# Optimization experiments

Hardware: AMD Instinct MI355X
Metric: run time of the kernel (lower is better)

## Reference

```python
import jax, jax.numpy as jnp
import numpy as np

N, F_IN, R, H, U, B, E = 20000, 256, 8, 4, 64, 4, 320000
NEG_SLOPE = 0.2  # torch F.leaky_relu default is 0.01, but GAT/RGAT uses 0.2; source uses F.leaky_relu -> 0.01
LRELU_SLOPE = 0.01


def setup_inputs() -> dict:
    key = jax.random.key(0)
    ks = jax.random.split(key, 8)
    x = jax.random.normal(ks[0], (N, F_IN), dtype=jnp.float32)
    basis = jax.random.normal(ks[1], (B, F_IN, U), dtype=jnp.float32) * 0.05
    coeff = jax.random.normal(ks[2], (R * H, B), dtype=jnp.float32)
    attn_q = jax.random.normal(ks[3], (R, H, U), dtype=jnp.float32) * 0.1
    attn_k = jax.random.normal(ks[4], (R, H, U), dtype=jnp.float32) * 0.1
    src = jax.random.randint(ks[5], (E,), 0, N, dtype=jnp.int32)
    dst = jax.random.randint(ks[6], (E,), 0, N, dtype=jnp.int32)
    rel = jax.random.randint(ks[7], (E,), 0, R, dtype=jnp.int32)
    return {"x": x, "basis": basis, "coeff": coeff, "attn_q": attn_q,
            "attn_k": attn_k, "src": src, "dst": dst, "rel": rel}


def reference(x, basis, coeff, attn_q, attn_k, src, dst, rel):
    n = x.shape[0]
    # Basis-decomposed relational kernels: W_{r,h} = sum_b c_{(r,h),b} W'_b
    W = jnp.einsum("cb,bfu->cfu", coeff, basis).reshape(R, H, F_IN, U)
    # Relation/head-specific projections: [N, R, H, U]
    xp = jnp.einsum("nf,rhfu->nrhu", x, W)
    # GAT-style 'sum' attention, attention_units=1: scalar query/key per (node, r, h)
    q = jnp.einsum("nrhu,rhu->nrh", xp, attn_q)  # [N, R, H]
    k = jnp.einsum("nrhu,rhu->nrh", xp, attn_k)  # [N, R, H]
    # Per-edge logits, gathered along sparse support: [E, H]
    logit = jax.nn.leaky_relu(q[src, rel] + k[dst, rel], negative_slope=LRELU_SLOPE)
    # ARGAT: segment softmax per destination node across all relations/edges
    m = jax.ops.segment_max(logit, dst, num_segments=n)        # [N, H]
    m = jnp.where(jnp.isfinite(m), m, 0.0)
    ex = jnp.exp(logit - m[dst])                               # [E, H]
    denom = jax.ops.segment_sum(ex, dst, num_segments=n)       # [N, H]
    alpha = ex / jnp.maximum(denom[dst], 1e-16)                # [E, H]
    # Weighted scatter-aggregation of messages: [N, H, U]
    msg = xp[src, rel] * alpha[:, :, None]                     # [E, H, U]
    out = jax.ops.segment_sum(msg, dst, num_segments=n)
    # head_aggregation='mean', activation=None, use_bias=False
    return out.mean(axis=1)  # [N, U]
```

## Files before the change

### kernel.cpp

```cpp
#include <hip/hip_runtime.h>
#include <hip/hip_bf16.h>
#include <math.h>

#define F_IN    256
#define R_REL   8
#define H_HEADS 4
#define U_DIM   64
#define B_BASES 4
#define C_TOT   (R_REL * H_HEADS)
#define LRELU   0.01f
#define SLOT_CAP 64

typedef __attribute__((ext_vector_type(8))) short short8;
typedef __attribute__((ext_vector_type(4))) float f32x4;

__device__ __forceinline__ unsigned short f2bf(float f) {
    unsigned int u = __float_as_uint(f);
    u = (u + 0x7FFF + ((u >> 16) & 1)) >> 16;
    return (unsigned short)u;
}
__device__ __forceinline__ float bf2f_lo(unsigned int v) { return __uint_as_float(v << 16); }
__device__ __forceinline__ float bf2f_hi(unsigned int v) { return __uint_as_float(v & 0xFFFF0000u); }

__global__ __launch_bounds__(256) void prep_all(const float* __restrict__ x,
                                                unsigned short* __restrict__ xb,
                                                int total4,
                                                int* __restrict__ counts,
                                                int n_nodes,
                                                const float* __restrict__ basis,
                                                const float* __restrict__ coeff,
                                                const float* __restrict__ attn_q,
                                                const float* __restrict__ attn_k,
                                                unsigned short* __restrict__ Wt,
                                                int n_cast_blocks) {
    if (blockIdx.x < (unsigned)n_cast_blocks) {
        int i = blockIdx.x * 256 + threadIdx.x;
        if (i < n_nodes) counts[i] = 0;
        if (i >= total4) return;
        float4 v = *(const float4*)&x[(size_t)i * 4];
        ushort4 o;
        o.x = f2bf(v.x); o.y = f2bf(v.y); o.z = f2bf(v.z); o.w = f2bf(v.w);
        *(ushort4*)&xb[(size_t)i * 4] = o;
        return;
    }

    __shared__ float aq[64], ak[64];
    int c = blockIdx.x - n_cast_blocks;
    int f = threadIdx.x;
    if (f < 64) {
        aq[f] = attn_q[c * 64 + f];
        ak[f] = attn_k[c * 64 + f];
    }
    __syncthreads();

    #pragma unroll
    for (int j = 0; j < 8; ++j) {
        int nn = c * 8 + j;
        int b = nn & 3, u = nn >> 2;
        Wt[(size_t)nn * 256 + f] = f2bf(basis[(size_t)b * (F_IN * U_DIM) + (size_t)f * U_DIM + u]);
    }

    float sq = 0.f, sk = 0.f;
    #pragma unroll
    for (int b = 0; b < B_BASES; ++b) {
        float cb = coeff[c * 4 + b];
        const float* bp = basis + (size_t)b * (F_IN * U_DIM) + (size_t)f * U_DIM;
        float dq = 0.f, dk = 0.f;
        #pragma unroll
        for (int u = 0; u < 64; ++u) {
            float v = bp[u];
            dq += v * aq[u];
            dk += v * ak[u];
        }
        sq += cb * dq;
        sk += cb * dk;
    }
    Wt[(size_t)(256 + c) * 256 + f] = f2bf(sq);
    Wt[(size_t)(288 + c) * 256 + f] = f2bf(sk);
}

__global__ __launch_bounds__(256) void gemm_scatter(const unsigned short* __restrict__ xb,
                                                    const unsigned short* __restrict__ Wt,
                                                    unsigned short* __restrict__ zb,
                                                    float* __restrict__ qk,
                                                    const int* __restrict__ src,
                                                    const int* __restrict__ dst,
                                                    const int* __restrict__ rel,
                                                    int* __restrict__ counts,
                                                    unsigned int* __restrict__ slots,
                                                    int nrows, int E) {
    if (blockIdx.y == 5) {
        int stride = gridDim.x * 256;
        int base = blockIdx.x * 256 + threadIdx.x;
        #pragma unroll
        for (int j = 0; j < 8; ++j) {
            int i = base + j * stride;
            if (i < E) {
                int d = dst[i];
                int pos = atomicAdd(&counts[d], 1);
                if (pos < SLOT_CAP)
                    slots[(size_t)d * SLOT_CAP + pos] = (unsigned)src[i] | ((unsigned)rel[i] << 20);
            }
        }
        return;
    }

    __shared__ unsigned short Al[128 * 72];
    __shared__ unsigned short Bl[64 * 72];

    const int tid  = threadIdx.x;
    const int wave = tid >> 6;
    const int lane = tid & 63;
    const int wr   = wave >> 1;
    const int wc   = wave & 1;
    const int m0   = blockIdx.x * 128;
    const int bb   = blockIdx.y;
    const int l15  = lane & 15;
    const int quad = lane >> 4;

    f32x4 acc[4][2];
    #pragma unroll
    for (int t = 0; t < 4; ++t)
        #pragma unroll
        for (int s = 0; s < 2; ++s)
            acc[t][s] = (f32x4){0.f, 0.f, 0.f, 0.f};

    for (int k0 = 0; k0 < 256; k0 += 64) {
        #pragma unroll
        for (int p = 0; p < 4; ++p) {
            int idx = p * 256 + tid;
            int row = idx >> 3;
            int cg  = idx & 7;
            int gr  = m0 + row;
            uint4 v = make_uint4(0, 0, 0, 0);
            if (gr < nrows) v = *(const uint4*)&xb[(size_t)gr * 256 + k0 + cg * 8];
            *(uint4*)&Al[row * 72 + cg * 8] = v;
        }
        #pragma unroll
        for (int p = 0; p < 2; ++p) {
            int idx = p * 256 + tid;
            int row = idx >> 3;
            int cg  = idx & 7;
            uint4 v = *(const uint4*)&Wt[(size_t)(bb * 64 + row) * 256 + k0 + cg * 8];
            *(uint4*)&Bl[row * 72 + cg * 8] = v;
        }
        __syncthreads();

        #pragma unroll
        for (int ks = 0; ks < 64; ks += 32) {
            short8 bfr[2];
            #pragma unroll
            for (int s = 0; s < 2; ++s)
                bfr[s] = *(short8*)&Bl[(wc * 32 + s * 16 + l15) * 72 + ks + quad * 8];
            #pragma unroll
            for (int t = 0; t < 4; ++t) {
                short8 afr = *(short8*)&Al[(wr * 64 + t * 16 + l15) * 72 + ks + quad * 8];
                #pragma unroll
                for (int s = 0; s < 2; ++s)
                    acc[t][s] = __builtin_amdgcn_mfma_f32_16x16x32_bf16(afr, bfr[s], acc[t][s], 0, 0, 0);
            }
        }
        __syncthreads();
    }

    #pragma unroll
    for (int t = 0; t < 4; ++t) {
        #pragma unroll
        for (int s = 0; s < 2; ++s) {
            int c_local = wc * 32 + s * 16 + l15;
            #pragma unroll
            for (int reg = 0; reg < 4; ++reg) {
                int m = m0 + wr * 64 + t * 16 + quad * 4 + reg;
                if (m < nrows) {
                    float v = acc[t][s][reg];
                    if (bb < 4) zb[(size_t)m * 256 + bb * 64 + c_local] = f2bf(v);
                    else        qk[(size_t)m * 64 + c_local] = v;
                }
            }
        }
    }
}

__global__ __launch_bounds__(256) void agg_kernel(const unsigned short* __restrict__ zb,
                                                  const float* __restrict__ qk,
                                                  const float* __restrict__ coeff,
                                                  const unsigned int* __restrict__ slots,
                                                  const int* __restrict__ counts,
                                                  float* __restrict__ out,
                                                  int n_nodes) {
    __shared__ float cf[128];
    __shared__ float4 gsh[4][64];
    __shared__ int    ssh[4][64];
    if (threadIdx.x < 128) cf[threadIdx.x] = coeff[threadIdx.x];
    __syncthreads();

    int wv   = threadIdx.x >> 6;
    int n    = blockIdx.x * 4 + wv;
    int lane = threadIdx.x & 63;
    if (n >= n_nodes) return;

    int cnt = counts[n];
    if (cnt > SLOT_CAP) cnt = SLOT_CAP;
    const unsigned int* sl = slots + (size_t)n * SLOT_CAP;

    float e0 = 0.f, e1 = 0.f, e2 = 0.f, e3 = 0.f;
    int s_edge = 0, r_edge = 0;
    if (lane < cnt) {
        unsigned p = sl[lane];
        s_edge = (int)(p & 0xFFFFFu);
        r_edge = (int)(p >> 20);
        float4 q  = *(const float4*)&qk[(size_t)s_edge * 64 + r_edge * 4];
        float4 kv = *(const float4*)&qk[(size_t)n * 64 + 32 + r_edge * 4];
        float l0 = q.x + kv.x, l1 = q.y + kv.y, l2 = q.z + kv.z, l3 = q.w + kv.w;
        l0 = (l0 > 0.f) ? l0 : LRELU * l0;
        l1 = (l1 > 0.f) ? l1 : LRELU * l1;
        l2 = (l2 > 0.f) ? l2 : LRELU * l2;
        l3 = (l3 > 0.f) ? l3 : LRELU * l3;
        e0 = __expf(l0); e1 = __expf(l1); e2 = __expf(l2); e3 = __expf(l3);
    }
    float d0 = e0, d1 = e1, d2 = e2, d3 = e3;
    #pragma unroll
    for (int off = 32; off; off >>= 1) {
        d0 += __shfl_xor(d0, off);
        d1 += __shfl_xor(d1, off);
        d2 += __shfl_xor(d2, off);
        d3 += __shfl_xor(d3, off);
    }
    if (lane < cnt) {
        float a0 = e0 * ((d0 > 0.f) ? 0.25f / d0 : 0.f);
        float a1 = e1 * ((d1 > 0.f) ? 0.25f / d1 : 0.f);
        float a2 = e2 * ((d2 > 0.f) ? 0.25f / d2 : 0.f);
        float a3 = e3 * ((d3 > 0.f) ? 0.25f / d3 : 0.f);
        const float* c0 = &cf[(r_edge * 4 + 0) * 4];
        const float* c1 = &cf[(r_edge * 4 + 1) * 4];
        const float* c2 = &cf[(r_edge * 4 + 2) * 4];
        const float* c3 = &cf[(r_edge * 4 + 3) * 4];
        float4 g4;
        g4.x = a0 * c0[0] + a1 * c1[0] + a2 * c2[0] + a3 * c3[0];
        g4.y = a0 * c0[1] + a1 * c1[1] + a2 * c2[1] + a3 * c3[1];
        g4.z = a0 * c0[2] + a1 * c1[2] + a2 * c2[2] + a3 * c3[2];
        g4.w = a0 * c0[3] + a1 * c1[3] + a2 * c2[3] + a3 * c3[3];
        gsh[wv][lane] = g4;
        ssh[wv][lane] = s_edge;
    }

    int es = lane >> 3;
    int g  = lane & 7;
    float acc[4][2];
    #pragma unroll
    for (int v = 0; v < 4; ++v) { acc[v][0] = 0.f; acc[v][1] = 0.f; }

    for (int base = 0; base < cnt; base += 8) {
        int i = base + es;
        if (i < cnt) {
            float4 g4 = gsh[wv][i];
            int s = ssh[wv][i];
            const unsigned short* zr = zb + (size_t)s * 256 + g * 8;
            #pragma unroll
            for (int v = 0; v < 4; ++v) {
                uint4 z4 = *(const uint4*)(zr + v * 64);
                acc[v][0] += g4.x * bf2f_lo(z4.x) + g4.y * bf2f_hi(z4.x) +
                             g4.z * bf2f_lo(z4.y) + g4.w * bf2f_hi(z4.y);
                acc[v][1] += g4.x * bf2f_lo(z4.z) + g4.y * bf2f_hi(z4.z) +
                             g4.z * bf2f_lo(z4.w) + g4.w * bf2f_hi(z4.w);
            }
        }
    }

    #pragma unroll
    for (int v = 0; v < 4; ++v) {
        #pragma unroll
        for (int j = 0; j < 2; ++j) {
            acc[v][j] += __shfl_xor(acc[v][j], 8);
            acc[v][j] += __shfl_xor(acc[v][j], 16);
            acc[v][j] += __shfl_xor(acc[v][j], 32);
        }
    }
    if (es == 0) {
        #pragma unroll
        for (int v = 0; v < 4; ++v) {
            float2 o = make_float2(acc[v][0], acc[v][1]);
            *(float2*)&out[(size_t)n * 64 + v * 16 + g * 2] = o;
        }
    }
}

extern "C" void kernel_launch(void* const* d_in, const int* in_sizes, int n_in,
                              void* d_out, int out_size, void* d_ws, size_t ws_size,
                              hipStream_t stream) {
    const float* x      = (const float*)d_in[0];
    const float* basis  = (const float*)d_in[1];
    const float* coeff  = (const float*)d_in[2];
    const float* attn_q = (const float*)d_in[3];
    const float* attn_k = (const float*)d_in[4];
    const int*   src    = (const int*)d_in[5];
    const int*   dst    = (const int*)d_in[6];
    const int*   rel    = (const int*)d_in[7];
    float* out = (float*)d_out;

    const int n_nodes = in_sizes[0] / F_IN;
    const int E       = in_sizes[5];

    char* ws = (char*)d_ws;
    size_t off = 0;
    auto alloc = [&](size_t bytes) -> void* {
        void* p = ws + off;
        off += bytes;
        off = (off + 255) & ~(size_t)255;
        return p;
    };
    unsigned short* xb   = (unsigned short*)alloc((size_t)n_nodes * 256 * 2);
    unsigned short* Wt   = (unsigned short*)alloc((size_t)320 * 256 * 2);
    unsigned short* zb   = (unsigned short*)alloc((size_t)n_nodes * 256 * 2);
    float* qk            = (float*)alloc((size_t)n_nodes * 64 * 4);
    unsigned int* slots  = (unsigned int*)alloc((size_t)n_nodes * SLOT_CAP * 4);
    int* counts          = (int*)alloc((size_t)n_nodes * 4);

    const int total4 = n_nodes * 64;
    const int n_cast_blocks = (total4 + 255) / 256;

    prep_all<<<n_cast_blocks + C_TOT, 256, 0, stream>>>(
        x, xb, total4, counts, n_nodes, basis, coeff, attn_q, attn_k, Wt, n_cast_blocks);

    dim3 g2((n_nodes + 127) / 128, 6);
    gemm_scatter<<<g2, 256, 0, stream>>>(xb, Wt, zb, qk, src, dst, rel, counts, slots,
                                         n_nodes, E);

    agg_kernel<<<(n_nodes + 3) / 4, 256, 0, stream>>>(zb, qk, coeff, slots, counts, out, n_nodes);
}
```

Baseline: 139.5 us.

## Load MFMA operands directly from global memory instead of staging through LDS

Drops the shared-memory tiles and the __syncthreads barriers in the projection GEMM. Each wave now loads its A and B MFMA fragments straight from global memory via per-row pointers, with the K loop fully unrolled. This removes LDS write/read traffic and block barriers and frees LDS for occupancy. The cost is that A rows are re-read by both column waves and B by both row waves through the cache, and each lane issues 16-byte strided global loads rather than coalesced tile loads.

```diff
diff --git a/kernel.cpp b/kernel.cpp
--- a/kernel.cpp
+++ b/kernel.cpp
@@ -105,9 +105,6 @@
         return;
     }
 
-    __shared__ unsigned short Al[128 * 72];
-    __shared__ unsigned short Bl[64 * 72];
-
     const int tid  = threadIdx.x;
     const int wave = tid >> 6;
     const int lane = tid & 63;
@@ -118,6 +115,16 @@
     const int l15  = lane & 15;
     const int quad = lane >> 4;
 
+    const unsigned short* Aptr[4];
+    #pragma unroll
+    for (int t = 0; t < 4; ++t) {
+        int m = m0 + wr * 64 + t * 16 + l15;
+        if (m >= nrows) m = 0;
+        Aptr[t] = xb + (size_t)m * 256 + quad * 8;
+    }
+    const unsigned short* Bptr0 = Wt + (size_t)(bb * 64 + wc * 32 + l15) * 256 + quad * 8;
+    const unsigned short* Bptr1 = Bptr0 + 16 * 256;
+
     f32x4 acc[4][2];
     #pragma unroll
     for (int t = 0; t < 4; ++t)
@@ -125,42 +132,16 @@
         for (int s = 0; s < 2; ++s)
             acc[t][s] = (f32x4){0.f, 0.f, 0.f, 0.f};
 
-    for (int k0 = 0; k0 < 256; k0 += 64) {
-        #pragma unroll
-        for (int p = 0; p < 4; ++p) {
-            int idx = p * 256 + tid;
-            int row = idx >> 3;
-            int cg  = idx & 7;
-            int gr  = m0 + row;
-            uint4 v = make_uint4(0, 0, 0, 0);
-            if (gr < nrows) v = *(const uint4*)&xb[(size_t)gr * 256 + k0 + cg * 8];
-            *(uint4*)&Al[row * 72 + cg * 8] = v;
-        }
-        #pragma unroll
-        for (int p = 0; p < 2; ++p) {
-            int idx = p * 256 + tid;
-            int row = idx >> 3;
-            int cg  = idx & 7;
-            uint4 v = *(const uint4*)&Wt[(size_t)(bb * 64 + row) * 256 + k0 + cg * 8];
-            *(uint4*)&Bl[row * 72 + cg * 8] = v;
-        }
-        __syncthreads();
-
-        #pragma unroll
-        for (int ks = 0; ks < 64; ks += 32) {
-            short8 bfr[2];
-            #pragma unroll
-            for (int s = 0; s < 2; ++s)
-                bfr[s] = *(short8*)&Bl[(wc * 32 + s * 16 + l15) * 72 + ks + quad * 8];
-            #pragma unroll
-            for (int t = 0; t < 4; ++t) {
-                short8 afr = *(short8*)&Al[(wr * 64 + t * 16 + l15) * 72 + ks + quad * 8];
-                #pragma unroll
-                for (int s = 0; s < 2; ++s)
-                    acc[t][s] = __builtin_amdgcn_mfma_f32_16x16x32_bf16(afr, bfr[s], acc[t][s], 0, 0, 0);
-            }
-        }
-        __syncthreads();
+    #pragma unroll
+    for (int kk = 0; kk < 256; kk += 32) {
+        short8 b0 = *(const short8*)(Bptr0 + kk);
+        short8 b1 = *(const short8*)(Bptr1 + kk);
+        #pragma unroll
+        for (int t = 0; t < 4; ++t) {
+            short8 a = *(const short8*)(Aptr[t] + kk);
+            acc[t][0] = __builtin_amdgcn_mfma_f32_16x16x32_bf16(a, b0, acc[t][0], 0, 0, 0);
+            acc[t][1] = __builtin_amdgcn_mfma_f32_16x16x32_bf16(a, b1, acc[t][1], 0, 0, 0);
+        }
     }
 
     #pragma unroll
```

Result: slower. 145.7 us (+4.4%).

## Widen GEMM N-tile to 128, vectorize stores, fold edge scatter into qk blocks

Applied to the files above, without the earlier changes.

Changes the grid from 6 to 3 y-slices. The z projection now uses 128-column tiles (two y-slices instead of four), which halves how often the x tile is reloaded from global memory. The qk y-slice also runs the edge bucketing scatter after its GEMM. MFMA operands are swapped so each lane holds four consecutive output columns, which allows vectorized ushort4 and float4 stores. The trade-offs are higher register and LDS use, and serializing the scatter behind the qk GEMM, which lengthens those blocks and may make the load imbalanced.

```diff
diff --git a/kernel.cpp b/kernel.cpp
--- a/kernel.cpp
+++ b/kernel.cpp
@@ -79,34 +79,18 @@
     Wt[(size_t)(288 + c) * 256 + f] = f2bf(sk);
 }
 
-__global__ __launch_bounds__(256) void gemm_scatter(const unsigned short* __restrict__ xb,
-                                                    const unsigned short* __restrict__ Wt,
-                                                    unsigned short* __restrict__ zb,
-                                                    float* __restrict__ qk,
-                                                    const int* __restrict__ src,
-                                                    const int* __restrict__ dst,
-                                                    const int* __restrict__ rel,
-                                                    int* __restrict__ counts,
-                                                    unsigned int* __restrict__ slots,
-                                                    int nrows, int E) {
-    if (blockIdx.y == 5) {
-        int stride = gridDim.x * 256;
-        int base = blockIdx.x * 256 + threadIdx.x;
-        #pragma unroll
-        for (int j = 0; j < 8; ++j) {
-            int i = base + j * stride;
-            if (i < E) {
-                int d = dst[i];
-                int pos = atomicAdd(&counts[d], 1);
-                if (pos < SLOT_CAP)
-                    slots[(size_t)d * SLOT_CAP + pos] = (unsigned)src[i] | ((unsigned)rel[i] << 20);
-            }
-        }
-        return;
-    }
-
+__global__ __launch_bounds__(256) void gemm_fused(const unsigned short* __restrict__ xb,
+                                                  const unsigned short* __restrict__ Wt,
+                                                  unsigned short* __restrict__ zb,
+                                                  float* __restrict__ qk,
+                                                  const int* __restrict__ src,
+                                                  const int* __restrict__ dst,
+                                                  const int* __restrict__ rel,
+                                                  int* __restrict__ counts,
+                                                  unsigned int* __restrict__ slots,
+                                                  int nrows, int E) {
     __shared__ unsigned short Al[128 * 72];
-    __shared__ unsigned short Bl[64 * 72];
+    __shared__ unsigned short Bl[128 * 72];
 
     const int tid  = threadIdx.x;
     const int wave = tid >> 6;
@@ -118,65 +102,135 @@
     const int l15  = lane & 15;
     const int quad = lane >> 4;
 
-    f32x4 acc[4][2];
-    #pragma unroll
-    for (int t = 0; t < 4; ++t)
-        #pragma unroll
-        for (int s = 0; s < 2; ++s)
-            acc[t][s] = (f32x4){0.f, 0.f, 0.f, 0.f};
-
-    for (int k0 = 0; k0 < 256; k0 += 64) {
-        #pragma unroll
-        for (int p = 0; p < 4; ++p) {
-            int idx = p * 256 + tid;
-            int row = idx >> 3;
-            int cg  = idx & 7;
-            int gr  = m0 + row;
-            uint4 v = make_uint4(0, 0, 0, 0);
-            if (gr < nrows) v = *(const uint4*)&xb[(size_t)gr * 256 + k0 + cg * 8];
-            *(uint4*)&Al[row * 72 + cg * 8] = v;
-        }
-        #pragma unroll
-        for (int p = 0; p < 2; ++p) {
-            int idx = p * 256 + tid;
-            int row = idx >> 3;
-            int cg  = idx & 7;
-            uint4 v = *(const uint4*)&Wt[(size_t)(bb * 64 + row) * 256 + k0 + cg * 8];
-            *(uint4*)&Bl[row * 72 + cg * 8] = v;
-        }
-        __syncthreads();
-
-        #pragma unroll
-        for (int ks = 0; ks < 64; ks += 32) {
-            short8 bfr[2];
+    if (bb < 2) {
+        f32x4 acc[4][4];
+        #pragma unroll
+        for (int t = 0; t < 4; ++t)
+            #pragma unroll
+            for (int s = 0; s < 4; ++s)
+                acc[t][s] = (f32x4){0.f, 0.f, 0.f, 0.f};
+
+        for (int k0 = 0; k0 < 256; k0 += 64) {
+            #pragma unroll
+            for (int p = 0; p < 4; ++p) {
+                int idx = p * 256 + tid;
+                int row = idx >> 3;
+                int cg  = idx & 7;
+                int gr  = m0 + row;
+                uint4 v = make_uint4(0, 0, 0, 0);
+                if (gr < nrows) v = *(const uint4*)&xb[(size_t)gr * 256 + k0 + cg * 8];
+                *(uint4*)&Al[row * 72 + cg * 8] = v;
+            }
+            #pragma unroll
+            for (int p = 0; p < 4; ++p) {
+                int idx = p * 256 + tid;
+                int row = idx >> 3;
+                int cg  = idx & 7;
+                uint4 v = *(const uint4*)&Wt[(size_t)(bb * 128 + row) * 256 + k0 + cg * 8];
+                *(uint4*)&Bl[row * 72 + cg * 8] = v;
+            }
+            __syncthreads();
+
+            #pragma unroll
+            for (int ks = 0; ks < 64; ks += 32) {
+                short8 wf[4];
+                #pragma unroll
+                for (int s = 0; s < 4; ++s)
+                    wf[s] = *(short8*)&Bl[(wc * 64 + s * 16 + l15) * 72 + ks + quad * 8];
+                #pragma unroll
+                for (int t = 0; t < 4; ++t) {
+                    short8 xf = *(short8*)&Al[(wr * 64 + t * 16 + l15) * 72 + ks + quad * 8];
+                    #pragma unroll
+                    for (int s = 0; s < 4; ++s)
+                        acc[t][s] = __builtin_amdgcn_mfma_f32_16x16x32_bf16(wf[s], xf, acc[t][s], 0, 0, 0);
+                }
+            }
+            __syncthreads();
+        }
+
+        #pragma unroll
+        for (int t = 0; t < 4; ++t) {
+            int m = m0 + wr * 64 + t * 16 + l15;
+            if (m < nrows) {
+                #pragma unroll
+                for (int s = 0; s < 4; ++s) {
+                    int c = bb * 128 + wc * 64 + s * 16 + quad * 4;
+                    ushort4 o;
+                    o.x = f2bf(acc[t][s][0]);
+                    o.y = f2bf(acc[t][s][1]);
+                    o.z = f2bf(acc[t][s][2]);
+                    o.w = f2bf(acc[t][s][3]);
+                    *(ushort4*)&zb[(size_t)m * 256 + c] = o;
+                }
+            }
+        }
+    } else {
+        f32x4 acc[4][2];
+        #pragma unroll
+        for (int t = 0; t < 4; ++t)
             #pragma unroll
             for (int s = 0; s < 2; ++s)
-                bfr[s] = *(short8*)&Bl[(wc * 32 + s * 16 + l15) * 72 + ks + quad * 8];
-            #pragma unroll
-            for (int t = 0; t < 4; ++t) {
-                short8 afr = *(short8*)&Al[(wr * 64 + t * 16 + l15) * 72 + ks + quad * 8];
+                acc[t][s] = (f32x4){0.f, 0.f, 0.f, 0.f};
+
+        for (int k0 = 0; k0 < 256; k0 += 64) {
+            #pragma unroll
+            for (int p = 0; p < 4; ++p) {
+                int idx = p * 256 + tid;
+                int row = idx >> 3;
+                int cg  = idx & 7;
+                int gr  = m0 + row;
+                uint4 v = make_uint4(0, 0, 0, 0);
+                if (gr < nrows) v = *(const uint4*)&xb[(size_t)gr * 256 + k0 + cg * 8];
+                *(uint4*)&Al[row * 72 + cg * 8] = v;
+            }
+            #pragma unroll
+            for (int p = 0; p < 2; ++p) {
+                int idx = p * 256 + tid;
+                int row = idx >> 3;
+                int cg  = idx & 7;
+                uint4 v = *(const uint4*)&Wt[(size_t)(256 + row) * 256 + k0 + cg * 8];
+                *(uint4*)&Bl[row * 72 + cg * 8] = v;
+            }
+            __syncthreads();
+
+            #pragma unroll
+            for (int ks = 0; ks < 64; ks += 32) {
+                short8 wf[2];
                 #pragma unroll
                 for (int s = 0; s < 2; ++s)
-                    acc[t][s] = __builtin_amdgcn_mfma_f32_16x16x32_bf16(afr, bfr[s], acc[t][s], 0, 0, 0);
-            }
-        }
-        __syncthreads();
-    }
-
-    #pragma unroll
-    for (int t = 0; t < 4; ++t) {
-        #pragma unroll
-        for (int s = 0; s < 2; ++s) {
-            int c_local = wc * 32 + s * 16 + l15;
-            #pragma unroll
-            for (int reg = 0; reg < 4; ++reg) {
-                int m = m0 + wr * 64 + t * 16 + quad * 4 + reg;
-                if (m < nrows) {
-                    float v = acc[t][s][reg];
-                    if (bb < 4) zb[(size_t)m * 256 + bb * 64 + c_local] = f2bf(v);
-                    else        qk[(size_t)m * 64 + c_local] = v;
+                    wf[s] = *(short8*)&Bl[(wc * 32 + s * 16 + l15) * 72 + ks + quad * 8];
+                #pragma unroll
+                for (int t = 0; t < 4; ++t) {
+                    short8 xf = *(short8*)&Al[(wr * 64 + t * 16 + l15) * 72 + ks + quad * 8];
+                    #pragma unroll
+                    for (int s = 0; s < 2; ++s)
+                        acc[t][s] = __builtin_amdgcn_mfma_f32_16x16x32_bf16(wf[s], xf, acc[t][s], 0, 0, 0);
                 }
             }
+            __syncthreads();
+        }
+
+        #pragma unroll
+        for (int t = 0; t < 4; ++t) {
+            int m = m0 + wr * 64 + t * 16 + l15;
+            if (m < nrows) {
+                #pragma unroll
+                for (int s = 0; s < 2; ++s) {
+                    int c = wc * 32 + s * 16 + quad * 4;
+                    float4 o = make_float4(acc[t][s][0], acc[t][s][1],
+                                           acc[t][s][2], acc[t][s][3]);
+                    *(float4*)&qk[(size_t)m * 64 + c] = o;
+                }
+            }
+        }
+
+        int stride = gridDim.x * 256;
+        int base = blockIdx.x * 256 + tid;
+        for (int i = base; i < E; i += stride) {
+            int d = dst[i];
+            int pos = atomicAdd(&counts[d], 1);
+            if (pos < SLOT_CAP)
+                slots[(size_t)d * SLOT_CAP + pos] = (unsigned)src[i] | ((unsigned)rel[i] << 20);
         }
     }
 }
@@ -322,9 +376,9 @@
     prep_all<<<n_cast_blocks + C_TOT, 256, 0, stream>>>(
         x, xb, total4, counts, n_nodes, basis, coeff, attn_q, attn_k, Wt, n_cast_blocks);
 
-    dim3 g2((n_nodes + 127) / 128, 6);
-    gemm_scatter<<<g2, 256, 0, stream>>>(xb, Wt, zb, qk, src, dst, rel, counts, slots,
-                                         n_nodes, E);
+    dim3 g2((n_nodes + 127) / 128, 3);
+    gemm_fused<<<g2, 256, 0, stream>>>(xb, Wt, zb, qk, src, dst, rel, counts, slots,
+                                       n_nodes, E);
 
     agg_kernel<<<(n_nodes + 3) / 4, 256, 0, stream>>>(zb, qk, coeff, slots, counts, out, n_nodes);
 }
```

New measurement: 146.4 us. +4.9%, slower.

## Split aggregation into two column-half passes with buffered edge weights

Applied to the files above, without the earlier changes.

The aggregation kernel is split into two launches. The first computes the softmax-derived per-edge basis weights, stores them to a global buffer, and accumulates output columns 0-31. The second reuses those stored weights to accumulate columns 32-63. This halves the gathered row footprint per pass, which is meant to improve cache locality of the zb gathers. In exchange it adds an extra launch, a global weight buffer written and re-read, and a second pass over the slot indices.

```diff
diff --git a/kernel.cpp b/kernel.cpp
--- a/kernel.cpp
+++ b/kernel.cpp
@@ -181,11 +181,12 @@
     }
 }
 
-__global__ __launch_bounds__(256) void agg_kernel(const unsigned short* __restrict__ zb,
+__global__ __launch_bounds__(256) void agg_phase0(const unsigned short* __restrict__ zb,
                                                   const float* __restrict__ qk,
                                                   const float* __restrict__ coeff,
                                                   const unsigned int* __restrict__ slots,
                                                   const int* __restrict__ counts,
+                                                  float4* __restrict__ gbuf,
                                                   float* __restrict__ out,
                                                   int n_nodes) {
     __shared__ float cf[128];
@@ -242,13 +243,13 @@
         g4.w = a0 * c0[3] + a1 * c1[3] + a2 * c2[3] + a3 * c3[3];
         gsh[wv][lane] = g4;
         ssh[wv][lane] = s_edge;
+        gbuf[(size_t)n * SLOT_CAP + lane] = g4;
     }
 
     int es = lane >> 3;
     int g  = lane & 7;
-    float acc[4][2];
-    #pragma unroll
-    for (int v = 0; v < 4; ++v) { acc[v][0] = 0.f; acc[v][1] = 0.f; }
+    float acc[2][2];
+    acc[0][0] = acc[0][1] = acc[1][0] = acc[1][1] = 0.f;
 
     for (int base = 0; base < cnt; base += 8) {
         int i = base + es;
@@ -257,7 +258,7 @@
             int s = ssh[wv][i];
             const unsigned short* zr = zb + (size_t)s * 256 + g * 8;
             #pragma unroll
-            for (int v = 0; v < 4; ++v) {
+            for (int v = 0; v < 2; ++v) {
                 uint4 z4 = *(const uint4*)(zr + v * 64);
                 acc[v][0] += g4.x * bf2f_lo(z4.x) + g4.y * bf2f_hi(z4.x) +
                              g4.z * bf2f_lo(z4.y) + g4.w * bf2f_hi(z4.y);
@@ -268,7 +269,7 @@
     }
 
     #pragma unroll
-    for (int v = 0; v < 4; ++v) {
+    for (int v = 0; v < 2; ++v) {
         #pragma unroll
         for (int j = 0; j < 2; ++j) {
             acc[v][j] += __shfl_xor(acc[v][j], 8);
@@ -278,9 +279,65 @@
     }
     if (es == 0) {
         #pragma unroll
-        for (int v = 0; v < 4; ++v) {
+        for (int v = 0; v < 2; ++v) {
             float2 o = make_float2(acc[v][0], acc[v][1]);
             *(float2*)&out[(size_t)n * 64 + v * 16 + g * 2] = o;
+        }
+    }
+}
+
+__global__ __launch_bounds__(256) void agg_phase1(const unsigned short* __restrict__ zb,
+                                                  const unsigned int* __restrict__ slots,
+                                                  const int* __restrict__ counts,
+                                                  const float4* __restrict__ gbuf,
+                                                  float* __restrict__ out,
+                                                  int n_nodes) {
+    int wv   = threadIdx.x >> 6;
+    int n    = blockIdx.x * 4 + wv;
+    int lane = threadIdx.x & 63;
+    if (n >= n_nodes) return;
+
+    int cnt = counts[n];
+    if (cnt > SLOT_CAP) cnt = SLOT_CAP;
+    const unsigned int* sl = slots + (size_t)n * SLOT_CAP;
+    const float4* gb = gbuf + (size_t)n * SLOT_CAP;
+
+    int es = lane >> 3;
+    int g  = lane & 7;
+    float acc[2][2];
+    acc[0][0] = acc[0][1] = acc[1][0] = acc[1][1] = 0.f;
+
+    for (int base = 0; base < cnt; base += 8) {
+        int i = base + es;
+        if (i < cnt) {
+            float4 g4 = gb[i];
+            int s = (int)(sl[i] & 0xFFFFFu);
+            const unsigned short* zr = zb + (size_t)s * 256 + 128 + g * 8;
+            #pragma unroll
+            for (int v = 0; v < 2; ++v) {
+                uint4 z4 = *(const uint4*)(zr + v * 64);
+                acc[v][0] += g4.x * bf2f_lo(z4.x) + g4.y * bf2f_hi(z4.x) +
+                             g4.z * bf2f_lo(z4.y) + g4.w * bf2f_hi(z4.y);
+                acc[v][1] += g4.x * bf2f_lo(z4.z) + g4.y * bf2f_hi(z4.z) +
+                             g4.z * bf2f_lo(z4.w) + g4.w * bf2f_hi(z4.w);
+            }
+        }
+    }
+
+    #pragma unroll
+    for (int v = 0; v < 2; ++v) {
+        #pragma unroll
+        for (int j = 0; j < 2; ++j) {
+            acc[v][j] += __shfl_xor(acc[v][j], 8);
+            acc[v][j] += __shfl_xor(acc[v][j], 16);
+            acc[v][j] += __shfl_xor(acc[v][j], 32);
+        }
+    }
+    if (es == 0) {
+        #pragma unroll
+        for (int v = 0; v < 2; ++v) {
+            float2 o = make_float2(acc[v][0], acc[v][1]);
+            *(float2*)&out[(size_t)n * 64 + 32 + v * 16 + g * 2] = o;
         }
     }
 }
@@ -314,6 +371,7 @@
     unsigned short* zb   = (unsigned short*)alloc((size_t)n_nodes * 256 * 2);
     float* qk            = (float*)alloc((size_t)n_nodes * 64 * 4);
     unsigned int* slots  = (unsigned int*)alloc((size_t)n_nodes * SLOT_CAP * 4);
+    float4* gbuf         = (float4*)alloc((size_t)n_nodes * SLOT_CAP * 16);
     int* counts          = (int*)alloc((size_t)n_nodes * 4);
 
     const int total4 = n_nodes * 64;
@@ -326,5 +384,7 @@
     gemm_scatter<<<g2, 256, 0, stream>>>(xb, Wt, zb, qk, src, dst, rel, counts, slots,
                                          n_nodes, E);
 
-    agg_kernel<<<(n_nodes + 3) / 4, 256, 0, stream>>>(zb, qk, coeff, slots, counts, out, n_nodes);
-}
+    agg_phase0<<<(n_nodes + 3) / 4, 256, 0, stream>>>(zb, qk, coeff, slots, counts,
+                                                      gbuf, out, n_nodes);
+    agg_phase1<<<(n_nodes + 3) / 4, 256, 0, stream>>>(zb, slots, counts, gbuf, out, n_nodes);
+}
```

New measurement: 143.0 us. 2.5% more time.
